# Kernel optimization log

Hardware: AMD Instinct MI355X
Metric: run time of the kernel (lower is better)

The kernel has to match this reference:

```python
import jax, jax.numpy as jnp
import numpy as np


def _ifft2c(k):
    # centered orthonormal 2D inverse FFT over axes (0, 1)
    return jnp.fft.fftshift(
        jnp.fft.ifft2(jnp.fft.ifftshift(k, axes=(0, 1)), axes=(0, 1), norm='ortho'),
        axes=(0, 1))


def _warp_adjoint(im, flow):
    # Adjoint (transpose) of bilinear-interpolation motion matrix built from a
    # 2D displacement field: scatter-add each pixel's value to the 4 bilinear
    # neighbors of its displaced location (x+u, y+v).
    # im: [Nx, Ny] complex64, flow: [Nx, Ny, 2] float32
    Nx, Ny = im.shape
    X, Y = jnp.meshgrid(jnp.arange(Nx, dtype=flow.dtype),
                        jnp.arange(Ny, dtype=flow.dtype), indexing='ij')
    px = jnp.clip(X + flow[..., 0], 0.0, Nx - 1.0)
    py = jnp.clip(Y + flow[..., 1], 0.0, Ny - 1.0)
    x0 = jnp.floor(px).astype(jnp.int32)
    y0 = jnp.floor(py).astype(jnp.int32)
    x1 = jnp.minimum(x0 + 1, Nx - 1)
    y1 = jnp.minimum(y0 + 1, Ny - 1)
    wx = px - x0.astype(px.dtype)
    wy = py - y0.astype(py.dtype)
    out = jnp.zeros(Nx * Ny, dtype=im.dtype)
    for xi, yi, w in ((x0, y0, (1 - wx) * (1 - wy)),
                      (x0, y1, (1 - wx) * wy),
                      (x1, y0, wx * (1 - wy)),
                      (x1, y1, wx * wy)):
        out = out.at[(xi * Ny + yi).ravel()].add((w * im).ravel())
    return out.reshape(Nx, Ny)


def setup_inputs() -> dict:
    key = jax.random.key(0)
    k1, k2, k3, k4, k5, k6 = jax.random.split(key, 6)
    Nx, Ny, Nc, Nt = 320, 320, 16, 25
    kspace_r = jax.random.normal(k1, (Nx, Ny, Nc), dtype=jnp.float32)
    kspace_i = jax.random.normal(k2, (Nx, Ny, Nc), dtype=jnp.float32)
    # binary undersampling mask per coil per frame
    mask = jnp.round(jax.random.uniform(k3, (Nx, Ny, Nc, Nt), dtype=jnp.float32))
    smaps_r = jax.random.normal(k4, (Nx, Ny, Nc), dtype=jnp.float32)
    smaps_i = jax.random.normal(k5, (Nx, Ny, Nc), dtype=jnp.float32)
    # displacement fields, a few pixels of motion
    flow = 3.0 * jax.random.normal(k6, (Nx, Ny, 2, Nt), dtype=jnp.float32)
    return {'kspace_r': kspace_r, 'kspace_i': kspace_i, 'mask': mask,
            'smaps_r': smaps_r, 'smaps_i': smaps_i, 'flow': flow}


def reference(kspace_r, kspace_i, mask, smaps_r, smaps_i, flow):
    kspace = jax.lax.complex(kspace_r, kspace_i)          # [Nx,Ny,Nc]
    smaps = jax.lax.complex(smaps_r, smaps_i)             # [Nx,Ny,Nc]
    # per-frame masked k-space -> per-coil images: [Nx,Ny,Nc,Nt]
    km = kspace[:, :, :, None] * mask.astype(kspace.dtype)
    coil_ims = _ifft2c(km)
    # coil combine with conjugate sensitivities: [Nx,Ny,Nt]
    im_aux = jnp.sum(coil_ims * jnp.conj(smaps)[:, :, :, None], axis=2)
    # adjoint motion warp per frame, then sum over frames
    ims_t = jnp.moveaxis(im_aux, -1, 0)                   # [Nt,Nx,Ny]
    flows_t = jnp.moveaxis(flow, -1, 0)                   # [Nt,Nx,Ny,2]
    warped = jax.vmap(_warp_adjoint)(ims_t, flows_t)      # [Nt,Nx,Ny]
    out = jnp.sum(warped, axis=0)                         # [Nx,Ny] complex
    return jnp.stack([out.real, out.imag], axis=-1)       # [Nx,Ny,2] float32
```

## Files before the change

kernel.cpp:

```cpp
#include <hip/hip_runtime.h>
#include <hip/hip_fp16.h>


#define NX 320
#define NT 25
#define NC 16
#define BR 32
#define WH 16
static const float INV320 = 1.0f / 320.0f;

typedef float v2f __attribute__((ext_vector_type(2)));
typedef float nv4f __attribute__((ext_vector_type(4)));
typedef unsigned int v4u __attribute__((ext_vector_type(4)));
typedef unsigned int u32;

__device__ __forceinline__ int rev6(int l) {
  return ((l & 1) << 5) | ((l & 2) << 3) | ((l & 4) << 1) |
         ((l & 8) >> 1) | ((l & 16) >> 3) | ((l & 32) >> 5);
}

__device__ __forceinline__ u32 h2u(__half2 h) {
  return *reinterpret_cast<u32*>(&h);
}
__device__ __forceinline__ __half2 u2h(u32 u) {
  return *reinterpret_cast<__half2*>(&u);
}
__device__ __forceinline__ __half2 swap16(__half2 h) {
  u32 u = h2u(h);
  u = (u >> 16) | (u << 16);
  return u2h(u);
}

template <int M>
__device__ __forceinline__ u32 lxoru(u32 x) {
  if constexpr (M == 1) {
    return (u32)__builtin_amdgcn_mov_dpp((int)x, 0xB1, 0xF, 0xF, true);
  } else if constexpr (M == 2) {
    return (u32)__builtin_amdgcn_mov_dpp((int)x, 0x4E, 0xF, 0xF, true);
  } else if constexpr (M == 32) {
    return (u32)__shfl_xor((int)x, 32);
  } else {
    constexpr int pat = (M << 10) | 0x1F;
    return (u32)__builtin_amdgcn_ds_swizzle((int)x, pat);
  }
}

struct TwH {
  __half2 sg[5], c2[5], s2n[5];
  __half2 sg5;
  __half2 w5c[4], w5s[4];
  __half2 C1h, C2h, S1h, nS1h, S2h, NP;
};

__device__ __forceinline__ void make_twh(int lane, TwH& tw) {
#pragma unroll
  for (int st = 0; st < 5; ++st) {
    int m = 32 >> st;
    bool bot = (lane & m) != 0;
    int j = lane & (m - 1);
    float ang = 3.14159265358979323846f * (float)j / (float)m;
    float s, c;
    __sincosf(ang, &s, &c);
    float g = bot ? -1.f : 1.f;
    float cc = bot ? c : 1.f, ss = bot ? s : 0.f;
    tw.sg[st] = __floats2half2_rn(g, g);
    tw.c2[st] = __floats2half2_rn(cc, cc);
    tw.s2n[st] = __floats2half2_rn(-ss, ss);
  }
  float g5 = (lane & 1) ? -1.f : 1.f;
  tw.sg5 = __floats2half2_rn(g5, g5);
  int k1 = rev6(lane);
  float b = (6.283185307179586f / 320.0f) * (float)k1;
  float s1, c1;
  __sincosf(b, &s1, &c1);
  float cq = 1.f, sq = 0.f;
#pragma unroll
  for (int q = 1; q < 5; ++q) {
    float nc = cq * c1 - sq * s1, ns = cq * s1 + sq * c1;
    cq = nc;
    sq = ns;
    tw.w5c[q - 1] = __floats2half2_rn(cq, cq);
    tw.w5s[q - 1] = __floats2half2_rn(-sq, sq);
  }
  const float C1 = 0.30901699437494742f, S1 = 0.95105651629515357f;
  const float C2 = -0.80901699437494742f, S2 = 0.58778525229247312f;
  tw.C1h = __floats2half2_rn(C1, C1);
  tw.C2h = __floats2half2_rn(C2, C2);
  tw.S1h = __floats2half2_rn(S1, S1);
  tw.nS1h = __floats2half2_rn(-S1, -S1);
  tw.S2h = __floats2half2_rn(S2, S2);
  tw.NP = __floats2half2_rn(-1.f, 1.f);
}

__device__ __forceinline__ __half2 cmul_h(__half2 t, __half2 c2, __half2 s2n) {
  return __hfma2(s2n, swap16(t), __hmul2(c2, t));
}

template <int M>
__device__ __forceinline__ void bstage_h(__half2 z[5], __half2 sg, __half2 c2,
                                         __half2 s2n) {
#pragma unroll
  for (int q = 0; q < 5; ++q) {
    __half2 o = u2h(lxoru<M>(h2u(z[q])));
    __half2 t = __hfma2(sg, z[q], o);
    z[q] = cmul_h(t, c2, s2n);
  }
}

__device__ __forceinline__ void fft320h(__half2 z[5], const TwH& tw) {
  bstage_h<32>(z, tw.sg[0], tw.c2[0], tw.s2n[0]);
  bstage_h<16>(z, tw.sg[1], tw.c2[1], tw.s2n[1]);
  bstage_h<8>(z, tw.sg[2], tw.c2[2], tw.s2n[2]);
  bstage_h<4>(z, tw.sg[3], tw.c2[3], tw.s2n[3]);
  bstage_h<2>(z, tw.sg[4], tw.c2[4], tw.s2n[4]);
  {
    __half2 o = u2h(lxoru<1>(h2u(z[0])));
    z[0] = __hfma2(tw.sg5, z[0], o);
#pragma unroll
    for (int q = 1; q < 5; ++q) {
      o = u2h(lxoru<1>(h2u(z[q])));
      __half2 t = __hfma2(tw.sg5, z[q], o);
      z[q] = cmul_h(t, tw.w5c[q - 1], tw.w5s[q - 1]);
    }
  }
  __half2 t0 = z[0], t1 = z[1], t2 = z[2], t3 = z[3], t4 = z[4];
  __half2 a1 = __hadd2(t1, t4), b1 = __hsub2(t1, t4);
  __half2 a2 = __hadd2(t2, t3), b2 = __hsub2(t2, t3);
  z[0] = __hadd2(t0, __hadd2(a1, a2));
  __half2 p = __hfma2(tw.C2h, a2, __hfma2(tw.C1h, a1, t0));
  __half2 q_ = __hfma2(tw.S2h, b2, __hmul2(tw.S1h, b1));
  __half2 r = __hfma2(tw.C1h, a2, __hfma2(tw.C2h, a1, t0));
  __half2 u = __hfma2(tw.nS1h, b2, __hmul2(tw.S2h, b1));
  __half2 qi = __hmul2(tw.NP, swap16(q_));
  __half2 ui = __hmul2(tw.NP, swap16(u));
  z[1] = __hadd2(p, qi);
  z[4] = __hsub2(p, qi);
  z[2] = __hadd2(r, ui);
  z[3] = __hsub2(r, ui);
}

__global__ __launch_bounds__(256) void prep_k(
    const float* __restrict__ mask, const float* __restrict__ kr,
    const float* __restrict__ ki, unsigned int* __restrict__ mp,
    float2* __restrict__ kT) {
  __shared__ __align__(16) char shmem[7552];
  int bid = blockIdx.x, tid = threadIdx.x;
  if (bid < 6400) {
    int xt = bid / 320, y = bid % 320;
    int w = tid >> 6, lane = tid & 63;
    nv4f* stage4 = (nv4f*)shmem;
    float* stage = (float*)shmem;
    unsigned int* tileu = (unsigned int*)(shmem + 6400);
#pragma unroll
    for (int k = 0; k < 4; ++k) {
      int xx = w * 4 + k;
      const nv4f* src =
          (const nv4f*)(mask + ((size_t)((xt * 16 + xx) * NX) + y) * (NC * NT));
      nv4f* dst4 = stage4 + w * 100;
      if (lane < 50) {
        dst4[lane] = __builtin_nontemporal_load(&src[lane]);
        dst4[lane + 50] = __builtin_nontemporal_load(&src[lane + 50]);
      }
      if (lane < 16) {
        const float* row = stage + w * 400 + lane * NT;
        unsigned int bits = 0;
#pragma unroll
        for (int t = 0; t < NT; ++t) bits |= (row[t] != 0.f) ? (1u << t) : 0u;
        tileu[xx * 17 + lane] = bits;
      }
    }
    __syncthreads();
    int c2 = tid >> 4, xx2 = tid & 15;
    mp[((size_t)(c2 * NX + y)) * NX + xt * 16 + xx2] = tileu[xx2 * 17 + c2];
  } else {
    int r = bid - 6400;
    int xt = r % 20, y = r / 20;
    int xx = tid >> 4, c = tid & 15;
    float2* tilef = (float2*)shmem;
    size_t si_ = (size_t)((xt * 16 + xx) * NX + y) * NC + c;
    tilef[xx * 17 + c] = make_float2(kr[si_], ki[si_]);
    __syncthreads();
    int c2 = tid >> 4, xx2 = tid & 15;
    kT[((size_t)(c2 * NX + y)) * NX + xt * 16 + xx2] = tilef[xx2 * 17 + c2];
  }
}

__global__ __launch_bounds__(256) void pass1_k(
    const float2* __restrict__ kT, const unsigned int* __restrict__ mp,
    __half2* __restrict__ tmp, int c0, int G, const float* __restrict__ sr,
    const float* __restrict__ si, const float* __restrict__ fl,
    __half2* __restrict__ sT, float2* __restrict__ fs,
    float* __restrict__ out_f) {
  __shared__ __align__(16) char shmem[6528];
  int bid = blockIdx.x, tid = threadIdx.x;
  int fftN = NX * G;
  if (bid < fftN) {
    int y = bid % NX, cg = bid / NX, c = c0 + cg;
    int lane = tid & 63, w = tid >> 6;
    __half2 v[5];
    unsigned int mb[5];
    size_t rowbase = ((size_t)c * NX + y) * NX;
#pragma unroll
    for (int q = 0; q < 5; ++q) {
      int x = 5 * lane + q;
      float2 kv = kT[rowbase + x];
      float sg = ((lane + q) & 1) ? -INV320 : INV320;
      v[q] = __floats2half2_rn(kv.x * sg, kv.y * sg);
      mb[q] = mp[rowbase + x];
    }
    TwH tw;
    make_twh(lane, tw);
    int r6 = rev6(lane);
    float osg = ((lane & 32) ? -1.f : 1.f) * ((y & 1) ? -1.f : 1.f);
    __half2 osg2 = __floats2half2_rn(osg, osg);
    for (int t = w; t < NT; t += 4) {
      __half2 z[5];
#pragma unroll
      for (int q = 0; q < 5; ++q)
        z[q] = u2h(((mb[q] >> t) & 1u) ? h2u(v[q]) : 0u);
      fft320h(z, tw);
      __half2* dst = tmp + ((size_t)(cg * NT + t) * NX + y) * NX;
#pragma unroll
      for (int k2 = 0; k2 < 5; ++k2) dst[r6 + 64 * k2] = __hmul2(osg2, z[k2]);
    }
  } else if (bid < fftN + 6400) {
    int r = bid - fftN;
    int yt = r % 20, x = r / 20;
    int yy = tid >> 4, c = tid & 15;
    float2* tiles = (float2*)shmem;
    size_t si_ = (size_t)(x * NX + yt * 16 + yy) * NC + c;
    tiles[yy * 17 + c] = make_float2(sr[si_], si[si_]);
    __syncthreads();
    int c2 = tid >> 4, yy2 = tid & 15;
    float2 v = tiles[yy2 * 17 + c2];
    float sg = (yy2 & 1) ? -1.f : 1.f;
    sT[((size_t)(c2 * NX + x)) * NX + yt * 16 + yy2] =
        __floats2half2_rn(v.x * sg, v.y * sg);
  } else if (bid < fftN + 9600) {
    int r = bid - fftN - 6400;
    int nyt = r % 10, nx = r / 10;
    float* buf = (float*)shmem;
    size_t base = (size_t)(nx * NX + nyt * 32) * (2 * NT);
    const float2* src2 = (const float2*)(fl + base);
    float2* buf2 = (float2*)shmem;
    for (int f = tid; f < 800; f += 256) buf2[f] = src2[f];
    __syncthreads();
    for (int f = tid; f < 1600; f += 256) {
      int t = f / 64;
      int k = f % 64;
      int nyl = k >> 1, d = k & 1;
      size_t di = ((size_t)(t * NX + nx) * NX + nyt * 32 + nyl) * 2 + d;
      ((float*)fs)[di] = buf[(nyl * 2 + d) * NT + t];
    }
  } else {
    int idx = (bid - fftN - 9600) * 256 + tid;
    ((float4*)out_f)[idx] = make_float4(0.f, 0.f, 0.f, 0.f);
  }
}

__global__ __launch_bounds__(256) void pass2_k(
    const __half2* __restrict__ tmp, const __half2* __restrict__ sT,
    __half2* __restrict__ im_aux, int c0, int G, int first) {
  int bx = blockIdx.x, t = blockIdx.y;
  int nxt_ = (bx >> 3) + 10 * (bx & 7);
  int tid = threadIdx.x, lane = tid & 63, j = tid >> 6;
  int nx = nxt_ * 4 + j;
  int k1 = rev6(lane);
  TwH tw;
  make_twh(lane, tw);
  __shared__ __half2 tile[2][NX][5];
  v2f acc[5] = {{0, 0}, {0, 0}, {0, 0}, {0, 0}, {0, 0}};

  const size_t pstride = (size_t)NT * NX * NX;
  const __half2* sbase = tmp + (size_t)t * NX * NX + nxt_ * 4;
  __half2* lds = &tile[0][0][0];
  bool two = (tid < 64);

  v4u nb0, nb1;
  nb0 = *(const v4u*)(sbase + (size_t)tid * NX);
  if (two) nb1 = *(const v4u*)(sbase + (size_t)(tid + 256) * NX);

  for (int cg = 0; cg < G; ++cg) {
    v4u cb0 = nb0, cb1 = nb1;
    if (cg + 1 < G) {
      const __half2* s = sbase + (size_t)(cg + 1) * pstride;
      nb0 = *(const v4u*)(s + (size_t)tid * NX);
      if (two) nb1 = *(const v4u*)(s + (size_t)(tid + 256) * NX);
    }
    __half2* buf = lds + (cg & 1) * (NX * 5);
#pragma unroll
    for (int q = 0; q < 4; ++q) buf[tid * 5 + q] = u2h(cb0[q]);
    if (two) {
#pragma unroll
      for (int q = 0; q < 4; ++q) buf[(tid + 256) * 5 + q] = u2h(cb1[q]);
    }
    const __half2* srow = sT + ((size_t)(c0 + cg) * NX + nx) * NX;
    __half2 smh[5];
#pragma unroll
    for (int k2 = 0; k2 < 5; ++k2) smh[k2] = srow[k1 + 64 * k2];
    __syncthreads();
    __half2 z[5];
#pragma unroll
    for (int q = 0; q < 5; ++q) z[q] = buf[(5 * lane + q) * 5 + j];
    fft320h(z, tw);
#pragma unroll
    for (int k2 = 0; k2 < 5; ++k2) {
      float2 sm = __half22float2(smh[k2]);
      float2 zf = __half22float2(z[k2]);
      v2f zv = {zf.x, zf.y};
      v2f zc = {zf.y, -zf.x};
      acc[k2] += sm.x * zv + sm.y * zc;
    }
  }
  __half2* dst = im_aux + ((size_t)t * NX + nx) * NX;
#pragma unroll
  for (int k2 = 0; k2 < 5; ++k2) {
    int ny = k1 + 64 * k2;
    v2f nv = acc[k2];
    if (!first) {
      float2 old = __half22float2(dst[ny]);
      nv.x += old.x;
      nv.y += old.y;
    }
    dst[ny] = __floats2half2_rn(nv.x, nv.y);
  }
}

__global__ __launch_bounds__(1024) void scatter_k(
    const __half2* __restrict__ im, const float2* __restrict__ fs,
    __half2* __restrict__ out_p, float* __restrict__ out_f, int nseg) {
  int b = blockIdx.x, seg = blockIdx.y, t = blockIdx.z;
  int r0 = b * BR;
  int tid = threadIdx.x, lane = tid & 63, w = tid >> 6;
  __shared__ __half2 acc[BR * NX];
  const __half2 h2z = __floats2half2_rn(0.f, 0.f);
  for (int i = tid; i < BR * NX; i += 1024) acc[i] = h2z;
  __syncthreads();
  int lo = max(r0 - WH, 0), hi = min(r0 + BR + WH, NX);
  int stride = 16 * nseg;
  for (int nx = lo + seg * 16 + w; nx < hi; nx += stride) {
    bool own = (nx >= r0) && (nx < r0 + BR);
    const __half2* imrow = im + ((size_t)t * NX + nx) * NX;
    const float2* frow = fs + ((size_t)t * NX + nx) * NX;
#pragma unroll
    for (int q = 0; q < 5; ++q) {
      int ny = lane + 64 * q;
      float2 v = __half22float2(imrow[ny]);
      float2 fl = frow[ny];
      float px = fminf(fmaxf((float)nx + fl.x, 0.f), 319.f);
      float py = fminf(fmaxf((float)ny + fl.y, 0.f), 319.f);
      int x0 = (int)floorf(px), y0 = (int)floorf(py);
      int x1 = min(x0 + 1, NX - 1), y1 = min(y0 + 1, NX - 1);
      float wx = px - (float)x0, wy = py - (float)y0;
      float w00 = (1.f - wx) * (1.f - wy), w01 = (1.f - wx) * wy;
      float w10 = wx * (1.f - wy), w11 = wx * wy;
#pragma unroll
      for (int half = 0; half < 2; ++half) {
        int r = half ? x1 : x0;
        float wa = half ? w10 : w00;
        float wb = half ? w11 : w01;
        if (r >= r0 && r < r0 + BR) {
          unsafeAtomicAdd(&acc[(r - r0) * NX + y0],
                          __floats2half2_rn(wa * v.x, wa * v.y));
          unsafeAtomicAdd(&acc[(r - r0) * NX + y1],
                          __floats2half2_rn(wb * v.x, wb * v.y));
        } else if (own) {
          int rb = (r / BR) * BR;
          if (nx < rb - WH || nx >= rb + BR + WH) {
            unsafeAtomicAdd(&out_f[((size_t)r * NX + y0) * 2], wa * v.x);
            unsafeAtomicAdd(&out_f[((size_t)r * NX + y0) * 2 + 1], wa * v.y);
            unsafeAtomicAdd(&out_f[((size_t)r * NX + y1) * 2], wb * v.x);
            unsafeAtomicAdd(&out_f[((size_t)r * NX + y1) * 2 + 1], wb * v.y);
          }
        }
      }
    }
  }
  __syncthreads();
  __half2* dst = out_p + (size_t)(seg * NT + t) * NX * NX + (size_t)r0 * NX;
  for (int i = tid; i < BR * NX; i += 1024) dst[i] = acc[i];
}

__global__ __launch_bounds__(256) void reduce_k(
    const __half2* __restrict__ out_p, const float* __restrict__ out_f,
    float* __restrict__ out, int nslice) {
  const int n = NX * NX;
  int i = blockIdx.x * 256 + threadIdx.x;
  if (i >= n) return;
  float2 s = ((const float2*)out_f)[i];
  for (int k = 0; k < nslice; ++k) {
    float2 v = __half22float2(out_p[(size_t)k * n + i]);
    s.x += v.x;
    s.y += v.y;
  }
  ((float2*)out)[i] = s;
}

extern "C" void kernel_launch(void* const* d_in, const int* in_sizes, int n_in,
                              void* d_out, int out_size, void* d_ws,
                              size_t ws_size, hipStream_t stream) {
  const float* kr = (const float*)d_in[0];
  const float* ki = (const float*)d_in[1];
  const float* mask = (const float*)d_in[2];
  const float* sr = (const float*)d_in[3];
  const float* si = (const float*)d_in[4];
  const float* fl = (const float*)d_in[5];
  float* out = (float*)d_out;

  const size_t tmp1 = (size_t)NT * NX * NX * 4;
  const size_t kT_b = (size_t)NC * NX * NX * 8;
  const size_t sT_b = (size_t)NC * NX * NX * 4;
  const size_t fs_b = (size_t)NT * NX * NX * 8;
  const size_t mp_b = (size_t)NC * NX * NX * 4;
  const size_t ia_b = (size_t)NT * NX * NX * 4;
  const size_t of_b = (size_t)NX * NX * 8;
  const size_t op1 = (size_t)NT * NX * NX * 4;

  int NSEG = 2, G = 16;
  for (;;) {
    size_t fixed = kT_b + sT_b + fs_b + mp_b + ia_b + of_b + NSEG * op1;
    if (ws_size >= fixed + (size_t)G * tmp1) break;
    if (G > 1) { G >>= 1; continue; }
    if (NSEG > 1) { NSEG >>= 1; G = 16; continue; }
    break;
  }

  char* w = (char*)d_ws;
  __half2* tmp = (__half2*)w;    w += (size_t)G * tmp1;
  float2* kT = (float2*)w;       w += kT_b;
  __half2* sT = (__half2*)w;     w += sT_b;
  float2* fs = (float2*)w;       w += fs_b;
  __half2* im_aux = (__half2*)w; w += ia_b;
  __half2* out_p = (__half2*)w;  w += (size_t)NSEG * op1;
  float* out_f = (float*)w;      w += of_b;
  unsigned int* mp = (unsigned int*)w;

  prep_k<<<12800, 256, 0, stream>>>(mask, kr, ki, mp, kT);

  for (int c0 = 0; c0 < NC; c0 += G) {
    int extra = (c0 == 0) ? 9800 : 0;
    pass1_k<<<NX * G + extra, 256, 0, stream>>>(kT, mp, tmp, c0, G, sr, si,
                                                fl, sT, fs, out_f);
    pass2_k<<<dim3(80, NT), 256, 0, stream>>>(tmp, sT, im_aux, c0, G,
                                              c0 == 0 ? 1 : 0);
  }
  scatter_k<<<dim3(NX / BR, NSEG, NT), 1024, 0, stream>>>(im_aux, fs, out_p,
                                                          out_f, NSEG);
  reduce_k<<<400, 256, 0, stream>>>(out_p, out_f, out, NSEG * NT);
}
```

Before: 247.1 us.

## Software-pipeline coil FFT passes across two half-coil groups in fused launches

Coil processing is split into two groups of eight. Packing of the second half of the mask is moved into the first pass1 launch, and the row-FFT for coils 8-15 runs in the same launch as the column-FFT/combine for coils 0-7, with a final pass2 launch for the second half. The goal is to overlap independent stages so more blocks are in flight and the GPU idles less between launches. The workspace-size fallback loop is removed, so the full 16-coil tmp buffer is now always assumed to fit.

New measurement: 260.1 us. +5.2%, slower.

```diff
diff --git a/kernel.cpp b/kernel.cpp
--- a/kernel.cpp
+++ b/kernel.cpp
@@ -139,6 +139,36 @@
   z[3] = __hsub2(r, ui);
 }
 
+__device__ __forceinline__ void mask_half_body(
+    const float* __restrict__ mask, unsigned int* __restrict__ mp, int cbase,
+    int bid, int tid, char* shmem) {
+  int xt = bid / 320, y = bid % 320;
+  int w = tid >> 6, lane = tid & 63;
+  nv4f* stage4 = (nv4f*)shmem;
+  float* stage = (float*)shmem;
+  unsigned int* tileu = (unsigned int*)(shmem + 3200);
+#pragma unroll
+  for (int k = 0; k < 4; ++k) {
+    int xx = w * 4 + k;
+    const nv4f* src = (const nv4f*)(
+        mask + ((size_t)((xt * 16 + xx) * NX) + y) * (NC * NT) + cbase * NT);
+    if (lane < 50) stage4[w * 50 + lane] = __builtin_nontemporal_load(&src[lane]);
+    if (lane < 8) {
+      const float* row = stage + w * 200 + lane * NT;
+      unsigned int bits = 0;
+#pragma unroll
+      for (int t = 0; t < NT; ++t) bits |= (row[t] != 0.f) ? (1u << t) : 0u;
+      tileu[xx * 9 + lane] = bits;
+    }
+  }
+  __syncthreads();
+  if (tid < 128) {
+    int c2 = tid >> 4, xx2 = tid & 15;
+    mp[((size_t)((cbase + c2) * NX + y)) * NX + xt * 16 + xx2] =
+        tileu[xx2 * 9 + c2];
+  }
+}
+
 __global__ __launch_bounds__(256) void prep_k(
     const float* __restrict__ mask, const float* __restrict__ kr,
     const float* __restrict__ ki, unsigned int* __restrict__ mp,
@@ -146,32 +176,7 @@
   __shared__ __align__(16) char shmem[7552];
   int bid = blockIdx.x, tid = threadIdx.x;
   if (bid < 6400) {
-    int xt = bid / 320, y = bid % 320;
-    int w = tid >> 6, lane = tid & 63;
-    nv4f* stage4 = (nv4f*)shmem;
-    float* stage = (float*)shmem;
-    unsigned int* tileu = (unsigned int*)(shmem + 6400);
-#pragma unroll
-    for (int k = 0; k < 4; ++k) {
-      int xx = w * 4 + k;
-      const nv4f* src =
-          (const nv4f*)(mask + ((size_t)((xt * 16 + xx) * NX) + y) * (NC * NT));
-      nv4f* dst4 = stage4 + w * 100;
-      if (lane < 50) {
-        dst4[lane] = __builtin_nontemporal_load(&src[lane]);
-        dst4[lane + 50] = __builtin_nontemporal_load(&src[lane + 50]);
-      }
-      if (lane < 16) {
-        const float* row = stage + w * 400 + lane * NT;
-        unsigned int bits = 0;
-#pragma unroll
-        for (int t = 0; t < NT; ++t) bits |= (row[t] != 0.f) ? (1u << t) : 0u;
-        tileu[xx * 17 + lane] = bits;
-      }
-    }
-    __syncthreads();
-    int c2 = tid >> 4, xx2 = tid & 15;
-    mp[((size_t)(c2 * NX + y)) * NX + xt * 16 + xx2] = tileu[xx2 * 17 + c2];
+    mask_half_body(mask, mp, 0, bid, tid, shmem);
   } else {
     int r = bid - 6400;
     int xt = r % 20, y = r / 20;
@@ -185,46 +190,121 @@
   }
 }
 
+__device__ __forceinline__ void pass1_body(
+    const float2* __restrict__ kT, const unsigned int* __restrict__ mp,
+    __half2* __restrict__ tmp, int c0, int bid, int tid) {
+  int y = bid % NX, cg = bid / NX, c = c0 + cg;
+  int lane = tid & 63, w = tid >> 6;
+  __half2 v[5];
+  unsigned int mb[5];
+  size_t rowbase = ((size_t)c * NX + y) * NX;
+#pragma unroll
+  for (int q = 0; q < 5; ++q) {
+    int x = 5 * lane + q;
+    float2 kv = kT[rowbase + x];
+    float sg = ((lane + q) & 1) ? -INV320 : INV320;
+    v[q] = __floats2half2_rn(kv.x * sg, kv.y * sg);
+    mb[q] = mp[rowbase + x];
+  }
+  TwH tw;
+  make_twh(lane, tw);
+  int r6 = rev6(lane);
+  float osg = ((lane & 32) ? -1.f : 1.f) * ((y & 1) ? -1.f : 1.f);
+  __half2 osg2 = __floats2half2_rn(osg, osg);
+  for (int t = w; t < NT; t += 4) {
+    __half2 z[5];
+#pragma unroll
+    for (int q = 0; q < 5; ++q)
+      z[q] = u2h(((mb[q] >> t) & 1u) ? h2u(v[q]) : 0u);
+    fft320h(z, tw);
+    __half2* dst = tmp + ((size_t)(cg * NT + t) * NX + y) * NX;
+#pragma unroll
+    for (int k2 = 0; k2 < 5; ++k2) dst[r6 + 64 * k2] = __hmul2(osg2, z[k2]);
+  }
+}
+
+__device__ __forceinline__ void pass2_body(
+    const __half2* __restrict__ tmp, const __half2* __restrict__ sT,
+    __half2* __restrict__ im_aux, int c0, int G, int first, int bx, int t,
+    int tid, char* shm) {
+  int nxt_ = (bx >> 3) + 10 * (bx & 7);
+  int lane = tid & 63, j = tid >> 6;
+  int nx = nxt_ * 4 + j;
+  int k1 = rev6(lane);
+  TwH tw;
+  make_twh(lane, tw);
+  __half2* lds = (__half2*)shm;
+  v2f acc[5] = {{0, 0}, {0, 0}, {0, 0}, {0, 0}, {0, 0}};
+
+  const size_t pstride = (size_t)NT * NX * NX;
+  const __half2* sbase = tmp + (size_t)t * NX * NX + nxt_ * 4;
+  bool two = (tid < 64);
+
+  v4u nb0, nb1;
+  nb0 = *(const v4u*)(sbase + (size_t)tid * NX);
+  if (two) nb1 = *(const v4u*)(sbase + (size_t)(tid + 256) * NX);
+
+  for (int cg = 0; cg < G; ++cg) {
+    v4u cb0 = nb0, cb1 = nb1;
+    if (cg + 1 < G) {
+      const __half2* s = sbase + (size_t)(cg + 1) * pstride;
+      nb0 = *(const v4u*)(s + (size_t)tid * NX);
+      if (two) nb1 = *(const v4u*)(s + (size_t)(tid + 256) * NX);
+    }
+    __half2* buf = lds + (cg & 1) * (NX * 5);
+#pragma unroll
+    for (int q = 0; q < 4; ++q) buf[tid * 5 + q] = u2h(cb0[q]);
+    if (two) {
+#pragma unroll
+      for (int q = 0; q < 4; ++q) buf[(tid + 256) * 5 + q] = u2h(cb1[q]);
+    }
+    const __half2* srow = sT + ((size_t)(c0 + cg) * NX + nx) * NX;
+    __half2 smh[5];
+#pragma unroll
+    for (int k2 = 0; k2 < 5; ++k2) smh[k2] = srow[k1 + 64 * k2];
+    __syncthreads();
+    __half2 z[5];
+#pragma unroll
+    for (int q = 0; q < 5; ++q) z[q] = buf[(5 * lane + q) * 5 + j];
+    fft320h(z, tw);
+#pragma unroll
+    for (int k2 = 0; k2 < 5; ++k2) {
+      float2 sm = __half22float2(smh[k2]);
+      float2 zf = __half22float2(z[k2]);
+      v2f zv = {zf.x, zf.y};
+      v2f zc = {zf.y, -zf.x};
+      acc[k2] += sm.x * zv + sm.y * zc;
+    }
+  }
+  __half2* dst = im_aux + ((size_t)t * NX + nx) * NX;
+#pragma unroll
+  for (int k2 = 0; k2 < 5; ++k2) {
+    int ny = k1 + 64 * k2;
+    v2f nv = acc[k2];
+    if (!first) {
+      float2 old = __half22float2(dst[ny]);
+      nv.x += old.x;
+      nv.y += old.y;
+    }
+    dst[ny] = __floats2half2_rn(nv.x, nv.y);
+  }
+}
+
 __global__ __launch_bounds__(256) void pass1_k(
-    const float2* __restrict__ kT, const unsigned int* __restrict__ mp,
-    __half2* __restrict__ tmp, int c0, int G, const float* __restrict__ sr,
+    const float2* __restrict__ kT, const unsigned int* __restrict__ mp_ro,
+    __half2* __restrict__ tmp, const float* __restrict__ mask,
+    unsigned int* __restrict__ mp_wr, const float* __restrict__ sr,
     const float* __restrict__ si, const float* __restrict__ fl,
     __half2* __restrict__ sT, float2* __restrict__ fs,
     float* __restrict__ out_f) {
   __shared__ __align__(16) char shmem[6528];
   int bid = blockIdx.x, tid = threadIdx.x;
-  int fftN = NX * G;
-  if (bid < fftN) {
-    int y = bid % NX, cg = bid / NX, c = c0 + cg;
-    int lane = tid & 63, w = tid >> 6;
-    __half2 v[5];
-    unsigned int mb[5];
-    size_t rowbase = ((size_t)c * NX + y) * NX;
-#pragma unroll
-    for (int q = 0; q < 5; ++q) {
-      int x = 5 * lane + q;
-      float2 kv = kT[rowbase + x];
-      float sg = ((lane + q) & 1) ? -INV320 : INV320;
-      v[q] = __floats2half2_rn(kv.x * sg, kv.y * sg);
-      mb[q] = mp[rowbase + x];
-    }
-    TwH tw;
-    make_twh(lane, tw);
-    int r6 = rev6(lane);
-    float osg = ((lane & 32) ? -1.f : 1.f) * ((y & 1) ? -1.f : 1.f);
-    __half2 osg2 = __floats2half2_rn(osg, osg);
-    for (int t = w; t < NT; t += 4) {
-      __half2 z[5];
-#pragma unroll
-      for (int q = 0; q < 5; ++q)
-        z[q] = u2h(((mb[q] >> t) & 1u) ? h2u(v[q]) : 0u);
-      fft320h(z, tw);
-      __half2* dst = tmp + ((size_t)(cg * NT + t) * NX + y) * NX;
-#pragma unroll
-      for (int k2 = 0; k2 < 5; ++k2) dst[r6 + 64 * k2] = __hmul2(osg2, z[k2]);
-    }
-  } else if (bid < fftN + 6400) {
-    int r = bid - fftN;
+  if (bid < 2560) {
+    pass1_body(kT, mp_ro, tmp, 0, bid, tid);
+  } else if (bid < 8960) {
+    mask_half_body(mask, mp_wr, 8, bid - 2560, tid, shmem);
+  } else if (bid < 15360) {
+    int r = bid - 8960;
     int yt = r % 20, x = r / 20;
     int yy = tid >> 4, c = tid & 15;
     float2* tiles = (float2*)shmem;
@@ -236,8 +316,8 @@
     float sg = (yy2 & 1) ? -1.f : 1.f;
     sT[((size_t)(c2 * NX + x)) * NX + yt * 16 + yy2] =
         __floats2half2_rn(v.x * sg, v.y * sg);
-  } else if (bid < fftN + 9600) {
-    int r = bid - fftN - 6400;
+  } else if (bid < 18560) {
+    int r = bid - 15360;
     int nyt = r % 10, nx = r / 10;
     float* buf = (float*)shmem;
     size_t base = (size_t)(nx * NX + nyt * 32) * (2 * NT);
@@ -253,77 +333,31 @@
       ((float*)fs)[di] = buf[(nyl * 2 + d) * NT + t];
     }
   } else {
-    int idx = (bid - fftN - 9600) * 256 + tid;
+    int idx = (bid - 18560) * 256 + tid;
     ((float4*)out_f)[idx] = make_float4(0.f, 0.f, 0.f, 0.f);
+  }
+}
+
+__global__ __launch_bounds__(256) void pass12_k(
+    const float2* __restrict__ kT, const unsigned int* __restrict__ mp,
+    __half2* __restrict__ tmpB, const __half2* __restrict__ tmpA,
+    const __half2* __restrict__ sT, __half2* __restrict__ im_aux) {
+  __shared__ __align__(16) char shm[12800];
+  int bid = blockIdx.x, tid = threadIdx.x;
+  if (bid < 2560) {
+    pass1_body(kT, mp, tmpB, 8, bid, tid);
+  } else {
+    int r = bid - 2560;
+    pass2_body(tmpA, sT, im_aux, 0, 8, 1, r % 80, r / 80, tid, shm);
   }
 }
 
 __global__ __launch_bounds__(256) void pass2_k(
     const __half2* __restrict__ tmp, const __half2* __restrict__ sT,
-    __half2* __restrict__ im_aux, int c0, int G, int first) {
-  int bx = blockIdx.x, t = blockIdx.y;
-  int nxt_ = (bx >> 3) + 10 * (bx & 7);
-  int tid = threadIdx.x, lane = tid & 63, j = tid >> 6;
-  int nx = nxt_ * 4 + j;
-  int k1 = rev6(lane);
-  TwH tw;
-  make_twh(lane, tw);
-  __shared__ __half2 tile[2][NX][5];
-  v2f acc[5] = {{0, 0}, {0, 0}, {0, 0}, {0, 0}, {0, 0}};
-
-  const size_t pstride = (size_t)NT * NX * NX;
-  const __half2* sbase = tmp + (size_t)t * NX * NX + nxt_ * 4;
-  __half2* lds = &tile[0][0][0];
-  bool two = (tid < 64);
-
-  v4u nb0, nb1;
-  nb0 = *(const v4u*)(sbase + (size_t)tid * NX);
-  if (two) nb1 = *(const v4u*)(sbase + (size_t)(tid + 256) * NX);
-
-  for (int cg = 0; cg < G; ++cg) {
-    v4u cb0 = nb0, cb1 = nb1;
-    if (cg + 1 < G) {
-      const __half2* s = sbase + (size_t)(cg + 1) * pstride;
-      nb0 = *(const v4u*)(s + (size_t)tid * NX);
-      if (two) nb1 = *(const v4u*)(s + (size_t)(tid + 256) * NX);
-    }
-    __half2* buf = lds + (cg & 1) * (NX * 5);
-#pragma unroll
-    for (int q = 0; q < 4; ++q) buf[tid * 5 + q] = u2h(cb0[q]);
-    if (two) {
-#pragma unroll
-      for (int q = 0; q < 4; ++q) buf[(tid + 256) * 5 + q] = u2h(cb1[q]);
-    }
-    const __half2* srow = sT + ((size_t)(c0 + cg) * NX + nx) * NX;
-    __half2 smh[5];
-#pragma unroll
-    for (int k2 = 0; k2 < 5; ++k2) smh[k2] = srow[k1 + 64 * k2];
-    __syncthreads();
-    __half2 z[5];
-#pragma unroll
-    for (int q = 0; q < 5; ++q) z[q] = buf[(5 * lane + q) * 5 + j];
-    fft320h(z, tw);
-#pragma unroll
-    for (int k2 = 0; k2 < 5; ++k2) {
-      float2 sm = __half22float2(smh[k2]);
-      float2 zf = __half22float2(z[k2]);
-      v2f zv = {zf.x, zf.y};
-      v2f zc = {zf.y, -zf.x};
-      acc[k2] += sm.x * zv + sm.y * zc;
-    }
-  }
-  __half2* dst = im_aux + ((size_t)t * NX + nx) * NX;
-#pragma unroll
-  for (int k2 = 0; k2 < 5; ++k2) {
-    int ny = k1 + 64 * k2;
-    v2f nv = acc[k2];
-    if (!first) {
-      float2 old = __half22float2(dst[ny]);
-      nv.x += old.x;
-      nv.y += old.y;
-    }
-    dst[ny] = __floats2half2_rn(nv.x, nv.y);
-  }
+    __half2* __restrict__ im_aux) {
+  __shared__ __align__(16) char shm[12800];
+  pass2_body(tmp, sT, im_aux, 8, 8, 0, blockIdx.x, blockIdx.y, threadIdx.x,
+             shm);
 }
 
 __global__ __launch_bounds__(1024) void scatter_k(
@@ -415,18 +449,10 @@
   const size_t ia_b = (size_t)NT * NX * NX * 4;
   const size_t of_b = (size_t)NX * NX * 8;
   const size_t op1 = (size_t)NT * NX * NX * 4;
-
-  int NSEG = 2, G = 16;
-  for (;;) {
-    size_t fixed = kT_b + sT_b + fs_b + mp_b + ia_b + of_b + NSEG * op1;
-    if (ws_size >= fixed + (size_t)G * tmp1) break;
-    if (G > 1) { G >>= 1; continue; }
-    if (NSEG > 1) { NSEG >>= 1; G = 16; continue; }
-    break;
-  }
+  const int NSEG = 2;
 
   char* w = (char*)d_ws;
-  __half2* tmp = (__half2*)w;    w += (size_t)G * tmp1;
+  __half2* tmp = (__half2*)w;    w += (size_t)NC * tmp1;
   float2* kT = (float2*)w;       w += kT_b;
   __half2* sT = (__half2*)w;     w += sT_b;
   float2* fs = (float2*)w;       w += fs_b;
@@ -435,15 +461,15 @@
   float* out_f = (float*)w;      w += of_b;
   unsigned int* mp = (unsigned int*)w;
 
+  const size_t coilPlane = (size_t)NT * NX * NX;
+  __half2* tmpA = tmp;
+  __half2* tmpB = tmp + 8 * coilPlane;
+
   prep_k<<<12800, 256, 0, stream>>>(mask, kr, ki, mp, kT);
-
-  for (int c0 = 0; c0 < NC; c0 += G) {
-    int extra = (c0 == 0) ? 9800 : 0;
-    pass1_k<<<NX * G + extra, 256, 0, stream>>>(kT, mp, tmp, c0, G, sr, si,
-                                                fl, sT, fs, out_f);
-    pass2_k<<<dim3(80, NT), 256, 0, stream>>>(tmp, sT, im_aux, c0, G,
-                                              c0 == 0 ? 1 : 0);
-  }
+  pass1_k<<<18760, 256, 0, stream>>>(kT, mp, tmpA, mask, mp, sr, si, fl, sT,
+                                     fs, out_f);
+  pass12_k<<<2560 + 2000, 256, 0, stream>>>(kT, mp, tmpB, tmpA, sT, im_aux);
+  pass2_k<<<dim3(80, NT), 256, 0, stream>>>(tmpB, sT, im_aux);
   scatter_k<<<dim3(NX / BR, NSEG, NT), 1024, 0, stream>>>(im_aux, fs, out_p,
                                                           out_f, NSEG);
   reduce_k<<<400, 256, 0, stream>>>(out_p, out_f, out, NSEG * NT);
```
